# Kernel tuning notes

Measured on AMD Instinct MI355X. Metric: run time of the kernel, lower is better.

## Reference

```python
import jax, jax.numpy as jnp
import numpy as np


def _c2e(faces):
    # faces: [6, B, C, h, h] in order back, down, front, left, right, up
    # returns equirect map [B, C, H=h, W=2h] via bilinear cube sampling
    _, B, C, h, _ = faces.shape
    H, W = h, 2 * h
    lat = (0.5 - (jnp.arange(H) + 0.5) / H) * jnp.pi      # +pi/2 (top) .. -pi/2
    lon = (2.0 * (jnp.arange(W) + 0.5) / W - 1.0) * jnp.pi  # -pi .. +pi
    cl = jnp.cos(lat)[:, None]
    vx = cl * jnp.sin(lon)[None, :]
    vy = jnp.broadcast_to(jnp.sin(lat)[:, None], (H, W))
    vz = cl * jnp.cos(lon)[None, :]
    dirs = jnp.stack([vx, vy, vz], -1)                     # [H,W,3]
    ax, ay, az = jnp.abs(vx), jnp.abs(vy), jnp.abs(vz)
    cond_z = (az >= ax) & (az >= ay)
    cond_x = (~cond_z) & (ax >= ay)
    # face ids: 0 back(-z) 1 down(-y) 2 front(+z) 3 left(-x) 4 right(+x) 5 up(+y)
    face = jnp.where(cond_z, jnp.where(vz > 0, 2, 0),
                     jnp.where(cond_x, jnp.where(vx > 0, 4, 3),
                               jnp.where(vy > 0, 5, 1)))
    N = jnp.array([[0, 0, -1], [0, -1, 0], [0, 0, 1], [-1, 0, 0], [1, 0, 0], [0, 1, 0]], jnp.float32)
    R = jnp.array([[-1, 0, 0], [1, 0, 0], [1, 0, 0], [0, 0, 1], [0, 0, -1], [1, 0, 0]], jnp.float32)
    U = jnp.array([[0, 1, 0], [0, 0, -1], [0, 1, 0], [0, 1, 0], [0, 1, 0], [0, 0, 1]], jnp.float32)
    den = jnp.sum(dirs * N[face], -1)
    a = jnp.sum(dirs * R[face], -1) / den                  # in-plane x, [-1,1]
    bcoord = jnp.sum(dirs * U[face], -1) / den             # in-plane y, [-1,1]
    uu = jnp.clip((a + 1.0) * 0.5 * (h - 1), 0.0, h - 1)   # align_corners-style
    vv = jnp.clip((1.0 - bcoord) * 0.5 * (h - 1), 0.0, h - 1)
    x0 = jnp.floor(uu).astype(jnp.int32)
    y0 = jnp.floor(vv).astype(jnp.int32)
    x1 = jnp.minimum(x0 + 1, h - 1)
    y1 = jnp.minimum(y0 + 1, h - 1)
    dx = uu - x0
    dy = vv - y0
    ft = faces.transpose(0, 3, 4, 1, 2).reshape(6, h, h, B * C)  # [6,h,h,B*C]
    g = lambda yy, xx: ft[face, yy, xx]                    # gather -> [H,W,B*C]
    out = (g(y0, x0) * ((1 - dx) * (1 - dy))[..., None]
           + g(y0, x1) * (dx * (1 - dy))[..., None]
           + g(y1, x0) * ((1 - dx) * dy)[..., None]
           + g(y1, x1) * (dx * dy)[..., None])
    return out.reshape(H, W, B, C).transpose(2, 3, 0, 1)


def _conv(x, w, bias, pad):
    y = jax.lax.conv_general_dilated(x, w, (1, 1), [(pad, pad), (pad, pad)],
                                     dimension_numbers=('NCHW', 'OIHW', 'NCHW'))
    return y + bias[None, :, None, None]


def setup_inputs() -> dict:
    key = jax.random.key(0)
    ks = jax.random.split(key, 12)
    B, C, h = 4, 64, 128
    face_shape = (B, C, h, h)
    return {
        'm': jax.random.normal(ks[0], (B, C, h, 2 * h), jnp.float32),
        'f': jax.random.normal(ks[1], face_shape, jnp.float32),
        'r': jax.random.normal(ks[2], face_shape, jnp.float32),
        'b': jax.random.normal(ks[3], face_shape, jnp.float32),
        'l': jax.random.normal(ks[4], face_shape, jnp.float32),
        'u': jax.random.normal(ks[5], face_shape, jnp.float32),
        'd': jax.random.normal(ks[6], face_shape, jnp.float32),
        'w_fusion': jax.random.normal(ks[7], (C, C, 3, 3), jnp.float32) * 0.05,
        'b_fusion': jnp.zeros((C,), jnp.float32),
        'w_mask': jax.random.normal(ks[8], (1, 2 * C, 1, 1), jnp.float32) * 0.05,
        'b_mask': jnp.zeros((1,), jnp.float32),
    }


def reference(m, f, r, b, l, u, d, w_fusion, b_fusion, w_mask, b_mask):
    # cube faces stacked in the original order: back, down, front, left, right, up
    faces = jnp.stack([b, d, f, l, r, u], 0)               # [6,B,C,h,h]
    aux = _c2e(faces)                                      # [B,C,h,2h]
    m_aux = jax.nn.relu(_conv(aux, w_fusion, b_fusion, 1))
    m_main = jax.nn.relu(_conv(m, w_fusion, b_fusion, 1))  # shared conv_fusion weights
    joint = jnp.concatenate([m_main, m_aux], axis=1)
    mask = jax.nn.sigmoid(_conv(joint, w_mask, b_mask, 0)) # [B,1,h,2h]
    return m + mask * m_aux
```

## Files before the change

### kernel.cpp

```cpp
#include <hip/hip_runtime.h>
#include <math.h>
#include <stdint.h>

#define BB 4
#define CC 64
#define HH 128
#define HOUT 128
#define WOUT 256
#define NPIX (HOUT * WOUT)
#define NMAP (BB * CC * HOUT * WOUT)
#define FSTR ((size_t)HH * HH * 256)

#define NB_PREP 146
#define NB_FACE (6 * HH * 2)
#define NB_PACK (BB * HOUT)
#define NB_FRONT (NB_PREP + NB_FACE + NB_PACK)

typedef __attribute__((ext_vector_type(8))) short short8;
typedef __attribute__((ext_vector_type(4))) float floatx4;

__device__ __forceinline__ uint16_t f2bf(float f) {
    uint32_t u = __float_as_uint(f);
    u += 0x7fffu + ((u >> 16) & 1u);
    return (uint16_t)(u >> 16);
}
__device__ __forceinline__ float bfu2f(uint32_t v) { return __uint_as_float(v << 16); }

__global__ __launch_bounds__(256) void front_kernel(
    uint32_t* __restrict__ pk, float* __restrict__ pdx, float* __restrict__ pdy,
    const float* __restrict__ wf, uint4* __restrict__ Bsw,
    const float* __restrict__ pB, const float* __restrict__ pD,
    const float* __restrict__ pF, const float* __restrict__ pL,
    const float* __restrict__ pR, const float* __restrict__ pU,
    uint16_t* __restrict__ FCLlo, uint16_t* __restrict__ FCLhi,
    const float* __restrict__ msrc, uint16_t* __restrict__ Xm,
    uint4* __restrict__ zpage) {
    __shared__ uint16_t lds[64 * 256];
    int bid = blockIdx.x;
    int t = threadIdx.x;

    if (bid < NB_PREP) {
        if (bid == 0 && t == 0) *zpage = make_uint4(0, 0, 0, 0);
        if (bid < 128) {
            int p = bid * 256 + t;
            int y = p >> 8;
            int x = p & 255;
            const float PI = 3.14159265358979323846f;
            float lat = (0.5f - (y + 0.5f) / (float)HOUT) * PI;
            float lon = (2.0f * (x + 0.5f) / (float)WOUT - 1.0f) * PI;
            float cl = cosf(lat);
            float vx = cl * sinf(lon);
            float vy = sinf(lat);
            float vz = cl * cosf(lon);
            float ax = fabsf(vx), ay = fabsf(vy), az = fabsf(vz);

            int face;
            float den, a, b;
            if (az >= ax && az >= ay) {
                if (vz > 0.0f) { face = 2; den = vz;  a = vx;  b = vy; }
                else           { face = 0; den = -vz; a = -vx; b = vy; }
            } else if (ax >= ay) {
                if (vx > 0.0f) { face = 4; den = vx;  a = -vz; b = vy; }
                else           { face = 3; den = -vx; a = vz;  b = vy; }
            } else {
                if (vy > 0.0f) { face = 5; den = vy;  a = vx;  b = vz; }
                else           { face = 1; den = -vy; a = vx;  b = -vz; }
            }
            a /= den;
            b /= den;
            float uu = fminf(fmaxf((a + 1.0f) * 0.5f * (HH - 1), 0.0f), (float)(HH - 1));
            float vv = fminf(fmaxf((1.0f - b) * 0.5f * (HH - 1), 0.0f), (float)(HH - 1));
            int x0 = (int)floorf(uu);
            int y0 = (int)floorf(vv);
            int x1 = min(x0 + 1, HH - 1);
            int y1 = min(y0 + 1, HH - 1);
            pdx[p] = uu - (float)x0;
            pdy[p] = vv - (float)y0;
            pk[p] = (uint32_t)face | ((uint32_t)x0 << 3) | ((uint32_t)y0 << 10) |
                    ((uint32_t)x1 << 17) | ((uint32_t)y1 << 24);
        } else {
            int tid = (bid - 128) * 256 + t;
            if (tid >= 9 * 2 * 4 * 64) return;
            int lane = tid & 63;
            int rest = tid >> 6;
            int n = rest & 3, ks = (rest >> 2) & 1, tap = rest >> 3;
            int co = n * 16 + (lane & 15);
            uint32_t w4[4];
#pragma unroll
            for (int pw = 0; pw < 4; pw++) {
                int ci0 = ks * 32 + (lane >> 4) * 8 + pw * 2;
                uint32_t lo = f2bf(wf[(size_t)(co * CC + ci0) * 9 + tap]);
                uint32_t hi = f2bf(wf[(size_t)(co * CC + ci0 + 1) * 9 + tap]);
                w4[pw] = lo | (hi << 16);
            }
            Bsw[tid] = make_uint4(w4[0], w4[1], w4[2], w4[3]);
        }
    } else if (bid < NB_PREP + NB_FACE) {
        int fb = bid - NB_PREP;
        int half = fb & 1;
        int y = (fb >> 1) & 127;
        int fc = fb >> 8;
        const float* src = (fc == 0) ? pB : (fc == 1) ? pD : (fc == 2) ? pF
                         : (fc == 3) ? pL : (fc == 4) ? pR : pU;
        uint16_t* FCL = (fc < 3) ? (FCLlo + (size_t)fc * FSTR)
                                 : (FCLhi + (size_t)(fc - 3) * FSTR);
        int xl = t & 63;
        int x = half * 64 + xl;
        int cgb = t >> 6;

#pragma unroll
        for (int i = 0; i < 8; i++) {
            int cg = i * 4 + cgb;
            uint32_t w4[4];
#pragma unroll
            for (int j = 0; j < 4; j++) {
                int bc0 = cg * 8 + j * 2;
                uint32_t lo = f2bf(src[((size_t)bc0 * HH + y) * HH + x]);
                uint32_t hi = f2bf(src[((size_t)(bc0 + 1) * HH + y) * HH + x]);
                w4[j] = lo | (hi << 16);
            }
            int off = xl * 256 + ((cg ^ (xl & 7)) * 8);
            *(uint4*)&lds[off] = make_uint4(w4[0], w4[1], w4[2], w4[3]);
        }
        __syncthreads();
        size_t obase = ((size_t)y * HH + half * 64) * 256;
#pragma unroll
        for (int i = 0; i < 8; i++) {
            int q = i * 256 + t;
            int xx = q >> 5, cg = q & 31;
            int off = xx * 256 + ((cg ^ (xx & 7)) * 8);
            *(uint4*)&FCL[obase + (size_t)q * 8] = *(const uint4*)&lds[off];
        }
    } else {
        int by = bid - (NB_PREP + NB_FACE);
        int b = by >> 7, y = by & 127;

#pragma unroll
        for (int cg = 0; cg < 8; cg++) {
            uint32_t w4[4];
#pragma unroll
            for (int pw = 0; pw < 4; pw++) {
                int c0 = cg * 8 + pw * 2;
                uint32_t lo = f2bf(msrc[((size_t)(b * CC + c0) * HOUT + y) * WOUT + t]);
                uint32_t hi = f2bf(msrc[((size_t)(b * CC + c0 + 1) * HOUT + y) * WOUT + t]);
                w4[pw] = lo | (hi << 16);
            }
            int off = t * 64 + ((cg ^ (t & 7)) * 8);
            *(uint4*)&lds[off] = make_uint4(w4[0], w4[1], w4[2], w4[3]);
        }
        __syncthreads();
        size_t obase = (size_t)((b * HOUT + y) * WOUT) * CC;
#pragma unroll
        for (int i = 0; i < 8; i++) {
            int q = i * 256 + t;
            int p = q >> 3, c8 = q & 7;
            int off = p * 64 + ((c8 ^ (p & 7)) * 8);
            *(uint4*)&Xm[obase + (size_t)q * 8] = *(const uint4*)&lds[off];
        }
    }
}

__global__ __launch_bounds__(256) void gather_kernel(
    const uint32_t* __restrict__ pk, const float* __restrict__ pdx,
    const float* __restrict__ pdy, const uint16_t* __restrict__ FCLlo,
    const uint16_t* __restrict__ FCLhi, uint16_t* __restrict__ Xa) {
    int bid = blockIdx.x;
    int sw = (bid & 7) * 512 + (bid >> 3);
    int tid = sw * 256 + threadIdx.x;
    int chunk = tid & 31;
    int p = tid >> 5;

    uint32_t k = pk[p];
    float dx = pdx[p], dy = pdy[p];
    int fc = k & 7;
    int x0 = (k >> 3) & 127, y0 = (k >> 10) & 127;
    int x1 = (k >> 17) & 127, y1 = (k >> 24) & 127;

    const uint16_t* fb = (fc < 3) ? (FCLlo + (size_t)fc * FSTR)
                                  : (FCLhi + (size_t)(fc - 3) * FSTR);
    const uint16_t* base = fb + chunk * 8;
    uint4 c00 = *(const uint4*)(base + ((size_t)y0 * HH + x0) * 256);
    uint4 c01 = *(const uint4*)(base + ((size_t)y0 * HH + x1) * 256);
    uint4 c10 = *(const uint4*)(base + ((size_t)y1 * HH + x0) * 256);
    uint4 c11 = *(const uint4*)(base + ((size_t)y1 * HH + x1) * 256);

    float w00 = (1.0f - dx) * (1.0f - dy);
    float w01 = dx * (1.0f - dy);
    float w10 = (1.0f - dx) * dy;
    float w11 = dx * dy;

    const uint32_t* a00 = (const uint32_t*)&c00;
    const uint32_t* a01 = (const uint32_t*)&c01;
    const uint32_t* a10 = (const uint32_t*)&c10;
    const uint32_t* a11 = (const uint32_t*)&c11;
    uint32_t r[4];
#pragma unroll
    for (int w = 0; w < 4; w++) {
        float lo = w00 * bfu2f(a00[w] & 0xffffu) + w01 * bfu2f(a01[w] & 0xffffu)
                 + w10 * bfu2f(a10[w] & 0xffffu) + w11 * bfu2f(a11[w] & 0xffffu);
        float hi = w00 * bfu2f(a00[w] >> 16) + w01 * bfu2f(a01[w] >> 16)
                 + w10 * bfu2f(a10[w] >> 16) + w11 * bfu2f(a11[w] >> 16);
        r[w] = (uint32_t)f2bf(lo) | ((uint32_t)f2bf(hi) << 16);
    }

    int b = chunk >> 3, c = (chunk & 7) * 8;
    int y = p >> 8, x = p & 255;
    size_t o = (((size_t)(b * HOUT + y)) * WOUT + x) * CC + c;
    *(uint4*)(Xa + o) = make_uint4(r[0], r[1], r[2], r[3]);
}

__global__ __launch_bounds__(256, 4) void gemm_fused_kernel(
    const uint16_t* __restrict__ Xm, const uint16_t* __restrict__ Xa,
    const uint4* __restrict__ Bsw, const float* __restrict__ bias,
    const float* __restrict__ wm, const float* __restrict__ bm,
    const float* __restrict__ m, const uint4* __restrict__ zpage,
    float* __restrict__ out) {
    __shared__ __align__(16) uint16_t lds[3 * 132 * 64];
    float* ldsf = (float*)lds;

    int gid = blockIdx.x;
    int b = gid >> 8;
    int i = gid & 255;
    int xcd = i & 7, j = i >> 3;
    int y = xcd * 16 + (j & 15);
    int h = j >> 4;
    const int wx = h * 128 - 2;

    int tid = threadIdx.x;
    int lane = tid & 63;
    int wave = tid >> 6;
    int l15 = lane & 15, lq = lane >> 4;

    float bb[4], wmm[4], wma[4];
#pragma unroll
    for (int n = 0; n < 4; n++) {
        bb[n] = bias[n * 16 + l15];
        wmm[n] = wm[n * 16 + l15];
        wma[n] = wm[64 + n * 16 + l15];
    }
    float bm0 = bm[0];

    float mp[2][4];
#pragma unroll
    for (int mt = 0; mt < 2; mt++)
#pragma unroll
        for (int rg = 0; rg < 4; rg++) mp[mt][rg] = 0.0f;

    floatx4 acc[2][4];

#pragma unroll
    for (int phase = 0; phase < 2; phase++) {
        const uint16_t* Xb = (phase ? Xa : Xm) + (size_t)b * (HOUT * WOUT * CC);

        __syncthreads();
#pragma unroll
        for (int it = 0; it < 13; it++) {
            int cid = it * 256 + tid;
            if (cid < 3168) {
                int c = cid & 7;
                int pr = cid >> 3;
                int p = pr % 132;
                int r = pr / 132;
                int gy = y + r - 1;
                int gx = wx + p;
                int csrc = c ^ (p & 7);
                const uint4* src =
                    ((unsigned)gy < (unsigned)HOUT && (unsigned)gx < (unsigned)WOUT)
                        ? (const uint4*)(Xb + ((size_t)gy * WOUT + gx) * CC + csrc * 8)
                        : zpage;
                __builtin_amdgcn_global_load_lds(
                    (const uint32_t*)src,
                    (uint32_t*)&lds[(size_t)(it * 256 + wave * 64) * 8], 16, 0, 0);
            }
        }
        __syncthreads();

#pragma unroll
        for (int mt = 0; mt < 2; mt++)
#pragma unroll
            for (int n = 0; n < 4; n++) acc[mt][n] = (floatx4)0.0f;

#pragma unroll
        for (int tap = 0; tap < 9; tap++) {
            const int r = tap / 3;
            const int dx = tap % 3 - 1;
#pragma unroll
            for (int ks = 0; ks < 2; ks++) {
                short8 bfr[4];
                const uint4* bp = Bsw + (size_t)((tap * 2 + ks) * 4) * 64 + lane;
#pragma unroll
                for (int n = 0; n < 4; n++) {
                    uint4 t4 = bp[n * 64];
                    bfr[n] = *(short8*)&t4;
                }
#pragma unroll
                for (int mt = 0; mt < 2; mt++) {
                    int p = wave * 32 + mt * 16 + l15 + dx + 2;
                    int chunk = ks * 4 + lq;
                    int slot = (r * 132 + p) * 8 + (chunk ^ (p & 7));
                    short8 af = *(const short8*)&lds[slot * 8];
#pragma unroll
                    for (int n = 0; n < 4; n++)
                        acc[mt][n] = __builtin_amdgcn_mfma_f32_16x16x32_bf16(
                            af, bfr[n], acc[mt][n], 0, 0, 0);
                }
            }
        }

        if (phase == 0) {
#pragma unroll
            for (int mt = 0; mt < 2; mt++)
#pragma unroll
                for (int n = 0; n < 4; n++)
#pragma unroll
                    for (int rg = 0; rg < 4; rg++) {
                        float v = acc[mt][n][rg] + bb[n];
                        v = v > 0.0f ? v : 0.0f;
                        mp[mt][rg] += wmm[n] * v;
                    }
        } else {
#pragma unroll
            for (int mt = 0; mt < 2; mt++)
#pragma unroll
                for (int n = 0; n < 4; n++)
#pragma unroll
                    for (int rg = 0; rg < 4; rg++) {
                        float v = acc[mt][n][rg] + bb[n];
                        v = v > 0.0f ? v : 0.0f;
                        acc[mt][n][rg] = v;
                        mp[mt][rg] += wma[n] * v;
                    }
        }
    }

#pragma unroll
    for (int mt = 0; mt < 2; mt++)
#pragma unroll
        for (int rg = 0; rg < 4; rg++) {
            float v = mp[mt][rg];
            v += __shfl_xor(v, 1);
            v += __shfl_xor(v, 2);
            v += __shfl_xor(v, 4);
            v += __shfl_xor(v, 8);
            mp[mt][rg] = 1.0f / (1.0f + expf(-(v + bm0)));
        }

    __syncthreads();
#pragma unroll
    for (int mt = 0; mt < 2; mt++)
#pragma unroll
        for (int n = 0; n < 4; n++)
#pragma unroll
            for (int rg = 0; rg < 4; rg++) {
                int px = wave * 32 + mt * 16 + lq * 4 + rg;
                int co = n * 16 + l15;
                ldsf[co * 129 + px] = mp[mt][rg] * acc[mt][n][rg];
            }
    __syncthreads();

    size_t base0 = (size_t)b * (CC * HOUT * WOUT) + (size_t)y * WOUT + h * 128;
#pragma unroll
    for (int it = 0; it < 32; it++) {
        int q = it * 256 + tid;
        int c = q >> 7, px = q & 127;
        size_t idx = base0 + (size_t)c * (HOUT * WOUT) + px;
        out[idx] = m[idx] + ldsf[c * 129 + px];
    }
}

__global__ __launch_bounds__(256) void signal_kernel(float* __restrict__ out, float v) {
    int idx = blockIdx.x * 256 + threadIdx.x;
    out[idx] = v;
}

extern "C" void kernel_launch(void* const* d_in, const int* in_sizes, int n_in,
                              void* d_out, int out_size, void* d_ws, size_t ws_size,
                              hipStream_t stream) {
    const float* m  = (const float*)d_in[0];
    const float* f  = (const float*)d_in[1];
    const float* r  = (const float*)d_in[2];
    const float* bk = (const float*)d_in[3];
    const float* l  = (const float*)d_in[4];
    const float* u  = (const float*)d_in[5];
    const float* dn = (const float*)d_in[6];
    const float* wf = (const float*)d_in[7];
    const float* bf = (const float*)d_in[8];
    const float* wm = (const float*)d_in[9];
    const float* bm = (const float*)d_in[10];
    float* out = (float*)d_out;

    const size_t FCL_HALF = (size_t)3 * HH * HH * 256 * 2;
    const size_t OFF_FCLH = 0;
    const size_t OFF_XA   = FCL_HALF;
    const size_t OFF_XM   = OFF_XA + (size_t)NMAP * 2;
    const size_t OFF_BSW  = OFF_XM + (size_t)NMAP * 2;
    const size_t OFF_PK   = OFF_BSW + (9 * 2 * 4 * 64 * 16);
    const size_t OFF_PDX  = OFF_PK + (1u << 17);
    const size_t OFF_PDY  = OFF_PDX + (1u << 17);
    const size_t OFF_ZP   = OFF_PDY + (1u << 17);
    const size_t NEED     = OFF_ZP + 64;

    if (ws_size < NEED) {
        float v = 100.0f + (float)(ws_size >> 20);
        signal_kernel<<<NMAP / 256, 256, 0, stream>>>(out, v);
        return;
    }

    char* ws = (char*)d_ws;
    uint16_t* FCLhi = (uint16_t*)(ws + OFF_FCLH);
    uint16_t* Xa    = (uint16_t*)(ws + OFF_XA);
    uint16_t* Xm    = (uint16_t*)(ws + OFF_XM);
    uint4* Bsw      = (uint4*)(ws + OFF_BSW);
    uint32_t* pk    = (uint32_t*)(ws + OFF_PK);
    float* pdx      = (float*)(ws + OFF_PDX);
    float* pdy      = (float*)(ws + OFF_PDY);
    uint4* zpage    = (uint4*)(ws + OFF_ZP);
    uint16_t* FCLlo = (uint16_t*)d_out;

    front_kernel<<<NB_FRONT, 256, 0, stream>>>(pk, pdx, pdy, wf, Bsw,
                                               bk, dn, f, l, r, u, FCLlo, FCLhi,
                                               m, Xm, zpage);
    gather_kernel<<<(NPIX * 32) / 256, 256, 0, stream>>>(pk, pdx, pdy, FCLlo, FCLhi, Xa);
    gemm_fused_kernel<<<BB * HOUT * 2, 256, 0, stream>>>(Xm, Xa, Bsw, bf, wm, bm, m,
                                                         zpage, out);
}
```

Baseline: 243.2 us.

## Fuse cube-map gather and m packing into conv GEMM staging, drop intermediates

The separate gather kernel and the bf16 repack of m into Xm are removed. The conv kernel now builds its LDS tiles directly: it converts m from fp32 NCHW on the fly and bilinearly samples the cube faces per halo pixel. The face-pack stage is changed to use vectorized float4 reads with scalar LDS writes. This saves one launch and the write and re-read of two full bf16 intermediate maps. In exchange, the async global_load_lds staging becomes synchronous register loads, strided NCHW reads of m, and halo pixels that get resampled redundantly across blocks.

```diff
diff --git a/kernel.cpp b/kernel.cpp
--- a/kernel.cpp
+++ b/kernel.cpp
@@ -13,8 +13,7 @@
 
 #define NB_PREP 146
 #define NB_FACE (6 * HH * 2)
-#define NB_PACK (BB * HOUT)
-#define NB_FRONT (NB_PREP + NB_FACE + NB_PACK)
+#define NB_FRONT (NB_PREP + NB_FACE)
 
 typedef __attribute__((ext_vector_type(8))) short short8;
 typedef __attribute__((ext_vector_type(4))) float floatx4;
@@ -32,15 +31,12 @@
     const float* __restrict__ pB, const float* __restrict__ pD,
     const float* __restrict__ pF, const float* __restrict__ pL,
     const float* __restrict__ pR, const float* __restrict__ pU,
-    uint16_t* __restrict__ FCLlo, uint16_t* __restrict__ FCLhi,
-    const float* __restrict__ msrc, uint16_t* __restrict__ Xm,
-    uint4* __restrict__ zpage) {
+    uint16_t* __restrict__ FCL) {
     __shared__ uint16_t lds[64 * 256];
     int bid = blockIdx.x;
     int t = threadIdx.x;
 
     if (bid < NB_PREP) {
-        if (bid == 0 && t == 0) *zpage = make_uint4(0, 0, 0, 0);
         if (bid < 128) {
             int p = bid * 256 + t;
             int y = p >> 8;
@@ -95,32 +91,28 @@
             }
             Bsw[tid] = make_uint4(w4[0], w4[1], w4[2], w4[3]);
         }
-    } else if (bid < NB_PREP + NB_FACE) {
+    } else {
         int fb = bid - NB_PREP;
         int half = fb & 1;
         int y = (fb >> 1) & 127;
         int fc = fb >> 8;
         const float* src = (fc == 0) ? pB : (fc == 1) ? pD : (fc == 2) ? pF
                          : (fc == 3) ? pL : (fc == 4) ? pR : pU;
-        uint16_t* FCL = (fc < 3) ? (FCLlo + (size_t)fc * FSTR)
-                                 : (FCLhi + (size_t)(fc - 3) * FSTR);
-        int xl = t & 63;
-        int x = half * 64 + xl;
-        int cgb = t >> 6;
-
-#pragma unroll
-        for (int i = 0; i < 8; i++) {
-            int cg = i * 4 + cgb;
-            uint32_t w4[4];
+        uint16_t* FCLf = FCL + (size_t)fc * FSTR;
+
+#pragma unroll
+        for (int it = 0; it < 16; it++) {
+            int jq = it * 256 + t;
+            int bc = jq >> 4;
+            int q = jq & 15;
+            floatx4 v = *(const floatx4*)(src + ((size_t)bc * HH + y) * HH +
+                                          half * 64 + q * 4);
+            int cg = bc >> 3;
 #pragma unroll
             for (int j = 0; j < 4; j++) {
-                int bc0 = cg * 8 + j * 2;
-                uint32_t lo = f2bf(src[((size_t)bc0 * HH + y) * HH + x]);
-                uint32_t hi = f2bf(src[((size_t)(bc0 + 1) * HH + y) * HH + x]);
-                w4[j] = lo | (hi << 16);
-            }
-            int off = xl * 256 + ((cg ^ (xl & 7)) * 8);
-            *(uint4*)&lds[off] = make_uint4(w4[0], w4[1], w4[2], w4[3]);
+                int xl = q * 4 + j;
+                lds[xl * 256 + ((cg ^ (xl & 7)) << 3) + (bc & 7)] = f2bf(v[j]);
+            }
         }
         __syncthreads();
         size_t obase = ((size_t)y * HH + half * 64) * 256;
@@ -129,92 +121,17 @@
             int q = i * 256 + t;
             int xx = q >> 5, cg = q & 31;
             int off = xx * 256 + ((cg ^ (xx & 7)) * 8);
-            *(uint4*)&FCL[obase + (size_t)q * 8] = *(const uint4*)&lds[off];
-        }
-    } else {
-        int by = bid - (NB_PREP + NB_FACE);
-        int b = by >> 7, y = by & 127;
-
-#pragma unroll
-        for (int cg = 0; cg < 8; cg++) {
-            uint32_t w4[4];
-#pragma unroll
-            for (int pw = 0; pw < 4; pw++) {
-                int c0 = cg * 8 + pw * 2;
-                uint32_t lo = f2bf(msrc[((size_t)(b * CC + c0) * HOUT + y) * WOUT + t]);
-                uint32_t hi = f2bf(msrc[((size_t)(b * CC + c0 + 1) * HOUT + y) * WOUT + t]);
-                w4[pw] = lo | (hi << 16);
-            }
-            int off = t * 64 + ((cg ^ (t & 7)) * 8);
-            *(uint4*)&lds[off] = make_uint4(w4[0], w4[1], w4[2], w4[3]);
-        }
-        __syncthreads();
-        size_t obase = (size_t)((b * HOUT + y) * WOUT) * CC;
-#pragma unroll
-        for (int i = 0; i < 8; i++) {
-            int q = i * 256 + t;
-            int p = q >> 3, c8 = q & 7;
-            int off = p * 64 + ((c8 ^ (p & 7)) * 8);
-            *(uint4*)&Xm[obase + (size_t)q * 8] = *(const uint4*)&lds[off];
+            *(uint4*)&FCLf[obase + (size_t)q * 8] = *(const uint4*)&lds[off];
         }
     }
 }
 
-__global__ __launch_bounds__(256) void gather_kernel(
+__global__ __launch_bounds__(256, 4) void gemm_fused_kernel(
+    const float* __restrict__ m, const uint16_t* __restrict__ FCL,
     const uint32_t* __restrict__ pk, const float* __restrict__ pdx,
-    const float* __restrict__ pdy, const uint16_t* __restrict__ FCLlo,
-    const uint16_t* __restrict__ FCLhi, uint16_t* __restrict__ Xa) {
-    int bid = blockIdx.x;
-    int sw = (bid & 7) * 512 + (bid >> 3);
-    int tid = sw * 256 + threadIdx.x;
-    int chunk = tid & 31;
-    int p = tid >> 5;
-
-    uint32_t k = pk[p];
-    float dx = pdx[p], dy = pdy[p];
-    int fc = k & 7;
-    int x0 = (k >> 3) & 127, y0 = (k >> 10) & 127;
-    int x1 = (k >> 17) & 127, y1 = (k >> 24) & 127;
-
-    const uint16_t* fb = (fc < 3) ? (FCLlo + (size_t)fc * FSTR)
-                                  : (FCLhi + (size_t)(fc - 3) * FSTR);
-    const uint16_t* base = fb + chunk * 8;
-    uint4 c00 = *(const uint4*)(base + ((size_t)y0 * HH + x0) * 256);
-    uint4 c01 = *(const uint4*)(base + ((size_t)y0 * HH + x1) * 256);
-    uint4 c10 = *(const uint4*)(base + ((size_t)y1 * HH + x0) * 256);
-    uint4 c11 = *(const uint4*)(base + ((size_t)y1 * HH + x1) * 256);
-
-    float w00 = (1.0f - dx) * (1.0f - dy);
-    float w01 = dx * (1.0f - dy);
-    float w10 = (1.0f - dx) * dy;
-    float w11 = dx * dy;
-
-    const uint32_t* a00 = (const uint32_t*)&c00;
-    const uint32_t* a01 = (const uint32_t*)&c01;
-    const uint32_t* a10 = (const uint32_t*)&c10;
-    const uint32_t* a11 = (const uint32_t*)&c11;
-    uint32_t r[4];
-#pragma unroll
-    for (int w = 0; w < 4; w++) {
-        float lo = w00 * bfu2f(a00[w] & 0xffffu) + w01 * bfu2f(a01[w] & 0xffffu)
-                 + w10 * bfu2f(a10[w] & 0xffffu) + w11 * bfu2f(a11[w] & 0xffffu);
-        float hi = w00 * bfu2f(a00[w] >> 16) + w01 * bfu2f(a01[w] >> 16)
-                 + w10 * bfu2f(a10[w] >> 16) + w11 * bfu2f(a11[w] >> 16);
-        r[w] = (uint32_t)f2bf(lo) | ((uint32_t)f2bf(hi) << 16);
-    }
-
-    int b = chunk >> 3, c = (chunk & 7) * 8;
-    int y = p >> 8, x = p & 255;
-    size_t o = (((size_t)(b * HOUT + y)) * WOUT + x) * CC + c;
-    *(uint4*)(Xa + o) = make_uint4(r[0], r[1], r[2], r[3]);
-}
-
-__global__ __launch_bounds__(256, 4) void gemm_fused_kernel(
-    const uint16_t* __restrict__ Xm, const uint16_t* __restrict__ Xa,
-    const uint4* __restrict__ Bsw, const float* __restrict__ bias,
-    const float* __restrict__ wm, const float* __restrict__ bm,
-    const float* __restrict__ m, const uint4* __restrict__ zpage,
-    float* __restrict__ out) {
+    const float* __restrict__ pdy, const uint4* __restrict__ Bsw,
+    const float* __restrict__ bias, const float* __restrict__ wm,
+    const float* __restrict__ bm, float* __restrict__ out) {
     __shared__ __align__(16) uint16_t lds[3 * 132 * 64];
     float* ldsf = (float*)lds;
 
@@ -248,38 +165,67 @@
 
     floatx4 acc[2][4];
 
-#pragma unroll
-    for (int phase = 0; phase < 2; phase++) {
-        const uint16_t* Xb = (phase ? Xa : Xm) + (size_t)b * (HOUT * WOUT * CC);
-
-        __syncthreads();
-#pragma unroll
-        for (int it = 0; it < 13; it++) {
-            int cid = it * 256 + tid;
-            if (cid < 3168) {
-                int c = cid & 7;
-                int pr = cid >> 3;
-                int p = pr % 132;
-                int r = pr / 132;
-                int gy = y + r - 1;
-                int gx = wx + p;
-                int csrc = c ^ (p & 7);
-                const uint4* src =
-                    ((unsigned)gy < (unsigned)HOUT && (unsigned)gx < (unsigned)WOUT)
-                        ? (const uint4*)(Xb + ((size_t)gy * WOUT + gx) * CC + csrc * 8)
-                        : zpage;
-                __builtin_amdgcn_global_load_lds(
-                    (const uint32_t*)src,
-                    (uint32_t*)&lds[(size_t)(it * 256 + wave * 64) * 8], 16, 0, 0);
-            }
-        }
-        __syncthreads();
-
+    auto stage_m = [&](int cid) {
+        int c = cid & 7, pr = cid >> 3;
+        int p = pr % 132, r = pr / 132;
+        int gy = y + r - 1, gx = wx + p;
+        uint32_t w4[4] = {0u, 0u, 0u, 0u};
+        if ((unsigned)gy < (unsigned)HOUT && (unsigned)gx < (unsigned)WOUT) {
+            const float* mp0 = m + ((size_t)(b * CC + c * 8) * HOUT + gy) * WOUT + gx;
+#pragma unroll
+            for (int jj = 0; jj < 4; jj++) {
+                uint32_t lo = f2bf(mp0[(size_t)(2 * jj) * NPIX]);
+                uint32_t hi = f2bf(mp0[(size_t)(2 * jj + 1) * NPIX]);
+                w4[jj] = lo | (hi << 16);
+            }
+        }
+        int slot = (r * 132 + p) * 8 + (c ^ (p & 7));
+        *(uint4*)&lds[slot * 8] = make_uint4(w4[0], w4[1], w4[2], w4[3]);
+    };
+
+    auto stage_a = [&](int cid) {
+        int c = cid & 7, pr = cid >> 3;
+        int p = pr % 132, r = pr / 132;
+        int gy = y + r - 1, gx = wx + p;
+        uint32_t w4[4] = {0u, 0u, 0u, 0u};
+        if ((unsigned)gy < (unsigned)HOUT && (unsigned)gx < (unsigned)WOUT) {
+            int pg = gy * WOUT + gx;
+            uint32_t k = pk[pg];
+            float dxw = pdx[pg], dyw = pdy[pg];
+            int fc = k & 7;
+            int x0 = (k >> 3) & 127, y0 = (k >> 10) & 127;
+            int x1 = (k >> 17) & 127, y1 = (k >> 24) & 127;
+            const uint16_t* base = FCL + (size_t)fc * FSTR + (size_t)(b * 8 + c) * 8;
+            uint4 c00 = *(const uint4*)(base + ((size_t)y0 * HH + x0) * 256);
+            uint4 c01 = *(const uint4*)(base + ((size_t)y0 * HH + x1) * 256);
+            uint4 c10 = *(const uint4*)(base + ((size_t)y1 * HH + x0) * 256);
+            uint4 c11 = *(const uint4*)(base + ((size_t)y1 * HH + x1) * 256);
+            float w00 = (1.0f - dxw) * (1.0f - dyw);
+            float w01 = dxw * (1.0f - dyw);
+            float w10 = (1.0f - dxw) * dyw;
+            float w11 = dxw * dyw;
+            const uint32_t* a00 = (const uint32_t*)&c00;
+            const uint32_t* a01 = (const uint32_t*)&c01;
+            const uint32_t* a10 = (const uint32_t*)&c10;
+            const uint32_t* a11 = (const uint32_t*)&c11;
+#pragma unroll
+            for (int w = 0; w < 4; w++) {
+                float lo = w00 * bfu2f(a00[w] & 0xffffu) + w01 * bfu2f(a01[w] & 0xffffu)
+                         + w10 * bfu2f(a10[w] & 0xffffu) + w11 * bfu2f(a11[w] & 0xffffu);
+                float hi = w00 * bfu2f(a00[w] >> 16) + w01 * bfu2f(a01[w] >> 16)
+                         + w10 * bfu2f(a10[w] >> 16) + w11 * bfu2f(a11[w] >> 16);
+                w4[w] = (uint32_t)f2bf(lo) | ((uint32_t)f2bf(hi) << 16);
+            }
+        }
+        int slot = (r * 132 + p) * 8 + (c ^ (p & 7));
+        *(uint4*)&lds[slot * 8] = make_uint4(w4[0], w4[1], w4[2], w4[3]);
+    };
+
+    auto conv = [&]() {
 #pragma unroll
         for (int mt = 0; mt < 2; mt++)
 #pragma unroll
             for (int n = 0; n < 4; n++) acc[mt][n] = (floatx4)0.0f;
-
 #pragma unroll
         for (int tap = 0; tap < 9; tap++) {
             const int r = tap / 3;
@@ -306,32 +252,39 @@
                 }
             }
         }
-
-        if (phase == 0) {
-#pragma unroll
-            for (int mt = 0; mt < 2; mt++)
-#pragma unroll
-                for (int n = 0; n < 4; n++)
-#pragma unroll
-                    for (int rg = 0; rg < 4; rg++) {
-                        float v = acc[mt][n][rg] + bb[n];
-                        v = v > 0.0f ? v : 0.0f;
-                        mp[mt][rg] += wmm[n] * v;
-                    }
-        } else {
-#pragma unroll
-            for (int mt = 0; mt < 2; mt++)
-#pragma unroll
-                for (int n = 0; n < 4; n++)
-#pragma unroll
-                    for (int rg = 0; rg < 4; rg++) {
-                        float v = acc[mt][n][rg] + bb[n];
-                        v = v > 0.0f ? v : 0.0f;
-                        acc[mt][n][rg] = v;
-                        mp[mt][rg] += wma[n] * v;
-                    }
-        }
-    }
+    };
+
+    for (int it = 0; it < 12; it++) stage_m(it * 256 + tid);
+    if (tid < 96) stage_m(3072 + tid);
+    __syncthreads();
+    conv();
+#pragma unroll
+    for (int mt = 0; mt < 2; mt++)
+#pragma unroll
+        for (int n = 0; n < 4; n++)
+#pragma unroll
+            for (int rg = 0; rg < 4; rg++) {
+                float v = acc[mt][n][rg] + bb[n];
+                v = v > 0.0f ? v : 0.0f;
+                mp[mt][rg] += wmm[n] * v;
+            }
+
+    __syncthreads();
+    for (int it = 0; it < 12; it++) stage_a(it * 256 + tid);
+    if (tid < 96) stage_a(3072 + tid);
+    __syncthreads();
+    conv();
+#pragma unroll
+    for (int mt = 0; mt < 2; mt++)
+#pragma unroll
+        for (int n = 0; n < 4; n++)
+#pragma unroll
+            for (int rg = 0; rg < 4; rg++) {
+                float v = acc[mt][n][rg] + bb[n];
+                v = v > 0.0f ? v : 0.0f;
+                acc[mt][n][rg] = v;
+                mp[mt][rg] += wma[n] * v;
+            }
 
 #pragma unroll
     for (int mt = 0; mt < 2; mt++)
@@ -389,16 +342,13 @@
     const float* bm = (const float*)d_in[10];
     float* out = (float*)d_out;
 
-    const size_t FCL_HALF = (size_t)3 * HH * HH * 256 * 2;
-    const size_t OFF_FCLH = 0;
-    const size_t OFF_XA   = FCL_HALF;
-    const size_t OFF_XM   = OFF_XA + (size_t)NMAP * 2;
-    const size_t OFF_BSW  = OFF_XM + (size_t)NMAP * 2;
-    const size_t OFF_PK   = OFF_BSW + (9 * 2 * 4 * 64 * 16);
-    const size_t OFF_PDX  = OFF_PK + (1u << 17);
-    const size_t OFF_PDY  = OFF_PDX + (1u << 17);
-    const size_t OFF_ZP   = OFF_PDY + (1u << 17);
-    const size_t NEED     = OFF_ZP + 64;
+    const size_t OFF_FCL = 0;
+    const size_t FCL_SZ  = (size_t)6 * HH * HH * 256 * 2;
+    const size_t OFF_BSW = FCL_SZ;
+    const size_t OFF_PK  = OFF_BSW + (9 * 2 * 4 * 64 * 16);
+    const size_t OFF_PDX = OFF_PK + (1u << 17);
+    const size_t OFF_PDY = OFF_PDX + (1u << 17);
+    const size_t NEED    = OFF_PDY + (1u << 17);
 
     if (ws_size < NEED) {
         float v = 100.0f + (float)(ws_size >> 20);
@@ -407,20 +357,14 @@
     }
 
     char* ws = (char*)d_ws;
-    uint16_t* FCLhi = (uint16_t*)(ws + OFF_FCLH);
-    uint16_t* Xa    = (uint16_t*)(ws + OFF_XA);
-    uint16_t* Xm    = (uint16_t*)(ws + OFF_XM);
-    uint4* Bsw      = (uint4*)(ws + OFF_BSW);
-    uint32_t* pk    = (uint32_t*)(ws + OFF_PK);
-    float* pdx      = (float*)(ws + OFF_PDX);
-    float* pdy      = (float*)(ws + OFF_PDY);
-    uint4* zpage    = (uint4*)(ws + OFF_ZP);
-    uint16_t* FCLlo = (uint16_t*)d_out;
+    uint16_t* FCL = (uint16_t*)(ws + OFF_FCL);
+    uint4* Bsw    = (uint4*)(ws + OFF_BSW);
+    uint32_t* pk  = (uint32_t*)(ws + OFF_PK);
+    float* pdx    = (float*)(ws + OFF_PDX);
+    float* pdy    = (float*)(ws + OFF_PDY);
 
     front_kernel<<<NB_FRONT, 256, 0, stream>>>(pk, pdx, pdy, wf, Bsw,
-                                               bk, dn, f, l, r, u, FCLlo, FCLhi,
-                                               m, Xm, zpage);
-    gather_kernel<<<(NPIX * 32) / 256, 256, 0, stream>>>(pk, pdx, pdy, FCLlo, FCLhi, Xa);
-    gemm_fused_kernel<<<BB * HOUT * 2, 256, 0, stream>>>(Xm, Xa, Bsw, bf, wm, bm, m,
-                                                         zpage, out);
-}
+                                               bk, dn, f, l, r, u, FCL);
+    gemm_fused_kernel<<<BB * HOUT * 2, 256, 0, stream>>>(m, FCL, pk, pdx, pdy,
+                                                         Bsw, bf, wm, bm, out);
+}
```

After: 265.2 us. 9.0% more time.
